# Optimization experiments

Hardware: AMD Instinct MI355X
Metric: run time of the kernel (lower is better)

The kernel has to match this reference:

```python
import jax, jax.numpy as jnp
import numpy as np

B, C, H, W = 8, 256, 128, 128
HEADS, WS = 8, 8
SHIFT = WS // 2  # type=='W' -> shift_size = window_size//2 in this repo
N = WS * WS


def _rel_pos_index(ws):
    coords = np.stack(np.meshgrid(np.arange(ws), np.arange(ws), indexing='ij')).reshape(2, -1)
    rel = (coords[:, :, None] - coords[:, None, :]).transpose(1, 2, 0)  # N,N,2
    rel[:, :, 0] += ws - 1
    rel[:, :, 1] += ws - 1
    rel[:, :, 0] *= 2 * ws - 1
    return rel.sum(-1)  # (N,N) ints in [0,(2ws-1)^2)


def _attn_mask(h, w, ws, shift):
    img = np.zeros((h, w), np.int32)
    cnt = 0
    for hs in (slice(0, -ws), slice(-ws, -shift), slice(-shift, None)):
        for wsl in (slice(0, -ws), slice(-ws, -shift), slice(-shift, None)):
            img[hs, wsl] = cnt
            cnt += 1
    m = img.reshape(h // ws, ws, w // ws, ws).transpose(0, 2, 1, 3).reshape(-1, ws * ws)
    diff = m[:, None, :] - m[:, :, None]
    return np.where(diff != 0, -100.0, 0.0).astype(np.float32)  # (nW,N,N)


def _ln(x, w, b, eps=1e-5):
    mu = jnp.mean(x, -1, keepdims=True)
    var = jnp.mean(jnp.square(x - mu), -1, keepdims=True)
    return (x - mu) * jax.lax.rsqrt(var + eps) * w + b


def setup_inputs() -> dict:
    key = jax.random.key(0)
    ks = jax.random.split(key, 10)
    s = 0.02
    return {
        'x': jax.random.normal(ks[0], (B, C, H, W), jnp.float32),
        'ln1_w': jnp.ones((C,), jnp.float32),
        'ln1_b': jnp.zeros((C,), jnp.float32),
        'qkv_w': jax.random.normal(ks[1], (3 * C, C), jnp.float32) * s,
        'qkv_b': jnp.zeros((3 * C,), jnp.float32),
        'rel_bias': jax.random.normal(ks[2], ((2 * WS - 1) ** 2, HEADS), jnp.float32) * s,
        'proj_w': jax.random.normal(ks[3], (C, C), jnp.float32) * s,
        'proj_b': jnp.zeros((C,), jnp.float32),
        'ln2_w': jnp.ones((C,), jnp.float32),
        'ln2_b': jnp.zeros((C,), jnp.float32),
        'fc1_w': jax.random.normal(ks[4], (4 * C, C), jnp.float32) * s,
        'fc1_b': jnp.zeros((4 * C,), jnp.float32),
        'fc2_w': jax.random.normal(ks[5], (C, 4 * C), jnp.float32) * s,
        'fc2_b': jnp.zeros((C,), jnp.float32),
    }


def reference(x, ln1_w, ln1_b, qkv_w, qkv_b, rel_bias, proj_w, proj_b,
              ln2_w, ln2_b, fc1_w, fc1_b, fc2_w, fc2_b):
    b, c, h, w = x.shape
    hd = c // HEADS
    scale = hd ** -0.5
    nW = (h // WS) * (w // WS)

    t = x.transpose(0, 2, 3, 1).reshape(b, h * w, c)  # b (hw) c
    shortcut = t
    t = _ln(t, ln1_w, ln1_b).reshape(b, h, w, c)
    t = jnp.roll(t, (-SHIFT, -SHIFT), axis=(1, 2))  # cyclic shift
    # window partition -> (b*nW, N, c)
    win = t.reshape(b, h // WS, WS, w // WS, WS, c).transpose(0, 1, 3, 2, 4, 5).reshape(b * nW, N, c)

    qkv = (win @ qkv_w.T + qkv_b).reshape(b * nW, N, 3, HEADS, hd).transpose(2, 0, 3, 1, 4)
    q, k, v = qkv[0], qkv[1], qkv[2]  # (b*nW, heads, N, hd)
    attn = jnp.einsum('bhnd,bhmd->bhnm', q * scale, k)
    rpi = jnp.asarray(_rel_pos_index(WS))
    bias = rel_bias[rpi.reshape(-1)].reshape(N, N, HEADS).transpose(2, 0, 1)  # (heads,N,N)
    attn = attn + bias[None]
    mask = jnp.asarray(_attn_mask(h, w, WS, SHIFT))  # (nW,N,N)
    attn = attn.reshape(b, nW, HEADS, N, N) + mask[None, :, None]
    attn = jax.nn.softmax(attn, axis=-1).reshape(b * nW, HEADS, N, N)
    out = jnp.einsum('bhnm,bhmd->bhnd', attn, v).transpose(0, 2, 1, 3).reshape(b * nW, N, c)
    out = out @ proj_w.T + proj_b
    # window reverse + reverse shift
    out = out.reshape(b, h // WS, w // WS, WS, WS, c).transpose(0, 1, 3, 2, 4, 5).reshape(b, h, w, c)
    out = jnp.roll(out, (SHIFT, SHIFT), axis=(1, 2)).reshape(b, h * w, c)

    t = shortcut + out
    h2 = _ln(t, ln2_w, ln2_b)
    h2 = jax.nn.gelu(h2 @ fc1_w.T + fc1_b)
    t = t + (h2 @ fc2_w.T + fc2_b)
    return t.reshape(b, h, w, c).transpose(0, 3, 1, 2)
```

## Files before the change

kernel.cpp:

```cpp
#include <hip/hip_runtime.h>
#include <cstdint>
#include <cstddef>

using f32x4 = __attribute__((ext_vector_type(4))) float;
using bf16x8 = __attribute__((ext_vector_type(8))) __bf16;
using u16x4 = __attribute__((ext_vector_type(4))) unsigned short;
using u16x8 = __attribute__((ext_vector_type(8))) unsigned short;

#define DEV __device__ __forceinline__

DEV unsigned short f2b(float f) {
  __bf16 h = (__bf16)f;
  return __builtin_bit_cast(unsigned short, h);
}
DEV float b2f(unsigned short u) {
  uint32_t w = ((uint32_t)u) << 16;
  return __builtin_bit_cast(float, w);
}

DEV void gload16(const unsigned short* g, unsigned short* l) {
  __builtin_amdgcn_global_load_lds(
      (const __attribute__((address_space(1))) void*)g,
      (__attribute__((address_space(3))) void*)l, 16, 0, 0);
}

DEV void waitv(int n) {
  switch (n) {
    case 0: asm volatile("s_waitcnt vmcnt(0)" ::: "memory"); break;
    case 2: asm volatile("s_waitcnt vmcnt(2)" ::: "memory"); break;
    case 8: asm volatile("s_waitcnt vmcnt(8)" ::: "memory"); break;
    default: asm volatile("s_waitcnt vmcnt(0)" ::: "memory"); break;
  }
}


__global__ void swin_cvt_all(const float* __restrict__ qkvw, const float* __restrict__ projw,
                             const float* __restrict__ fc1w, const float* __restrict__ fc2w,
                             unsigned short* __restrict__ wq, unsigned short* __restrict__ wp,
                             unsigned short* __restrict__ w1, unsigned short* __restrict__ w2,
                             const float* __restrict__ relb, float* __restrict__ bt) {
  int i = blockIdx.x * 256 + threadIdx.x;
  if (i < 196608) wq[i] = f2b(qkvw[i]);
  else if (i < 262144) wp[i - 196608] = f2b(projw[i - 196608]);
  else if (i < 524288) w1[i - 262144] = f2b(fc1w[i - 262144]);
  else if (i < 786432) w2[i - 524288] = f2b(fc2w[i - 524288]);
  else {
    int id = i - 786432;
    int m = id & 63, n = (id >> 6) & 63, head = (id >> 12) & 7, cls = id >> 15;
    bool eh = cls & 2, ew = cls & 1;
    int nh = n >> 3, nw = n & 7, mh = m >> 3, mw = m & 7;
    int rn = (eh ? ((nh >> 2) + 1) : 0) * 3 + (ew ? ((nw >> 2) + 1) : 0);
    int rm = (eh ? ((mh >> 2) + 1) : 0) * 3 + (ew ? ((mw >> 2) + 1) : 0);
    float v = relb[(size_t)((nh - mh + 7) * 15 + (nw - mw + 7)) * 8 + head];
    if (rn != rm) v -= 100.f;
    bt[id] = v;
  }
}

__global__ __launch_bounds__(256)
void swin_ln1win(const float* __restrict__ x,
                 const float* __restrict__ lw, const float* __restrict__ lb,
                 unsigned short* __restrict__ win, unsigned short* __restrict__ xb) {
  __shared__ float sh[512];
  __shared__ float mean_[128], rstd_[128];
  __shared__ unsigned short tile[128 * 260];
  int bh = blockIdx.x; int b = bh >> 7, h = bh & 127;
  int t = threadIdx.x;
  int w = t & 127, ch = t >> 7;
  const float* px = x + (((size_t)(b * 256 + ch * 128)) << 14) + (h << 7) + w;
  float s = 0.f, s2 = 0.f;
  for (int c = 0; c < 128; ++c) {
    float v = px[(size_t)c << 14];
    s += v; s2 += v * v;
    tile[w * 260 + ch * 128 + c] = f2b(v);
  }
  sh[t] = s; sh[256 + t] = s2;
  __syncthreads();
  if (ch == 0) {
    s += sh[t + 128]; s2 += sh[256 + t + 128];
    float mu = s * (1.f / 256.f);
    mean_[w] = mu;
    rstd_[w] = rsqrtf(s2 * (1.f / 256.f) - mu * mu + 1e-5f);
  }
  __syncthreads();
  int hp = (h + 124) & 127;
  int whh = hp >> 3, nh = hp & 7;
  int lg = t & 31, grp = t >> 5;
#pragma unroll
  for (int i = 0; i < 16; ++i) {
    int w2 = (i << 3) + grp;
    float mu = mean_[w2], rs = rstd_[w2];
    int wp_ = (w2 + 124) & 127;
    int wwc = wp_ >> 3, nw = wp_ & 7;
    size_t wt = (size_t)b * 256 + whh * 16 + wwc;
    int n = (nh << 3) + nw;
#pragma unroll
    for (int half = 0; half < 2; ++half) {
      int c = half * 128 + (lg << 2);
      u16x4 raw = *(const u16x4*)&tile[w2 * 260 + c];
      f32x4 lwv = *(const f32x4*)(lw + c);
      f32x4 lbv = *(const f32x4*)(lb + c);
      u16x4 o;
#pragma unroll
      for (int k = 0; k < 4; ++k)
        o[k] = f2b((b2f(raw[k]) - mu) * rs * lwv[k] + lbv[k]);
      *(u16x4*)&win[((wt << 6) + n) * 256 + c] = o;
      *(u16x4*)&xb[(((size_t)bh << 7) + w2) * 256 + c] = raw;
    }
  }
}

__global__ __launch_bounds__(512)
void swin_qkvattn(const unsigned short* __restrict__ win,
                  const unsigned short* __restrict__ wq,
                  const float* __restrict__ qkvb,
                  const float* __restrict__ btab,
                  unsigned short* __restrict__ attn_out) {
  __shared__ __align__(16) char L[133120];
  const int wt = blockIdx.x;
  const int t = threadIdx.x;
  const int lane = t & 63;
  const int head = t >> 6;
  const int cl = lane & 15, g = lane >> 4;

  {
    const unsigned short* src = win + (size_t)wt * 16384;
    int row = t >> 3;
    int sch = (t & 7) ^ (row & 7);
#pragma unroll
    for (int o = 0; o < 4; ++o)
      gload16(src + row * 256 + o * 64 + sch * 8,
              (unsigned short*)(L + o * 8192 + t * 16));
  }
  __syncthreads();

  f32x4 acc1[4][6] = {};
#pragma unroll
  for (int kt = 0; kt < 8; ++kt) {
    bf16x8 af[4], bf[6];
    const char* sub = L + (kt >> 1) * 8192;
    const int kc = (kt & 1) * 4 + g;
#pragma unroll
    for (int i = 0; i < 4; ++i) {
      int tok = i * 16 + cl;
      af[i] = *(const bf16x8*)(sub + tok * 128 + ((kc ^ (tok & 7)) * 16));
    }
#pragma unroll
    for (int j = 0; j < 6; ++j) {
      int col = (j >> 1) * 256 + head * 32 + (j & 1) * 16 + cl;
      bf[j] = *(const bf16x8*)(wq + (size_t)col * 256 + kt * 32 + g * 8);
    }
#pragma unroll
    for (int i = 0; i < 4; ++i)
#pragma unroll
      for (int j = 0; j < 6; ++j)
        acc1[i][j] = __builtin_amdgcn_mfma_f32_16x16x32_bf16(bf[j], af[i], acc1[i][j], 0, 0, 0);
  }

  char* hb = L + 32768 + head * 12544;
#pragma unroll
  for (int i = 0; i < 4; ++i) {
    int tok = i * 16 + cl;
#pragma unroll
    for (int j = 0; j < 6; ++j) {
      int p = j >> 1;
      int c32b = (j & 1) * 16 + (g << 2);
      f32x4 b4 = *(const f32x4*)(qkvb + p * 256 + head * 32 + c32b);
      if (p < 2) {
        u16x4 o;
#pragma unroll
        for (int r = 0; r < 4; ++r) {
          float v = acc1[i][j][r] + b4[r];
          if (p == 0) v *= 0.17677669529663687f;
          o[r] = f2b(v);
        }
        int chunk = ((j & 1) * 2 + (g >> 1)) ^ ((tok >> 1) & 3);
        *(u16x4*)(hb + p * 4096 + tok * 64 + chunk * 16 + (g & 1) * 8) = o;
      } else {
        unsigned short* vt = (unsigned short*)(hb + 8192);
#pragma unroll
        for (int r = 0; r < 4; ++r)
          vt[(c32b + r) * 68 + tok] = f2b(acc1[i][j][r] + b4[r]);
      }
    }
  }
  asm volatile("s_waitcnt lgkmcnt(0)" ::: "memory");
  __builtin_amdgcn_sched_barrier(0);

  bf16x8 qf[4], kf[4];
#pragma unroll
  for (int ni = 0; ni < 4; ++ni) {
    int tok = (ni << 4) + cl;
    int chunk = g ^ ((tok >> 1) & 3);
    qf[ni] = *(const bf16x8*)(hb + tok * 64 + chunk * 16);
    kf[ni] = *(const bf16x8*)(hb + 4096 + tok * 64 + chunk * 16);
  }
  f32x4 s[4][4] = {};
#pragma unroll
  for (int mi = 0; mi < 4; ++mi)
#pragma unroll
    for (int ni = 0; ni < 4; ++ni)
      s[mi][ni] = __builtin_amdgcn_mfma_f32_16x16x32_bf16(kf[mi], qf[ni], s[mi][ni], 0, 0, 0);

  int wi = wt & 255;
  int cls = (((wi >> 4) == 15) ? 2 : 0) + (((wi & 15) == 15) ? 1 : 0);
  const float* bt = btab + (((size_t)(cls << 3) + head) << 12);
#pragma unroll
  for (int ni = 0; ni < 4; ++ni) {
    int n = (ni << 4) + cl;
    float mx = -1e30f;
#pragma unroll
    for (int mi = 0; mi < 4; ++mi) {
      f32x4 bb = *(const f32x4*)&bt[n * 64 + (mi << 4) + (g << 2)];
#pragma unroll
      for (int r = 0; r < 4; ++r) {
        float v = s[mi][ni][r] + bb[r];
        s[mi][ni][r] = v;
        mx = fmaxf(mx, v);
      }
    }
    mx = fmaxf(mx, __shfl_xor(mx, 16));
    mx = fmaxf(mx, __shfl_xor(mx, 32));
    float sum = 0.f;
#pragma unroll
    for (int mi = 0; mi < 4; ++mi)
#pragma unroll
      for (int r = 0; r < 4; ++r) {
        float p = __expf(s[mi][ni][r] - mx);
        s[mi][ni][r] = p;
        sum += p;
      }
    sum += __shfl_xor(sum, 16);
    sum += __shfl_xor(sum, 32);
    float inv = __builtin_amdgcn_rcpf(sum);
#pragma unroll
    for (int mi = 0; mi < 4; ++mi) {
      u16x4 pk;
#pragma unroll
      for (int r = 0; r < 4; ++r) pk[r] = f2b(s[mi][ni][r] * inv);
      int chunk = (mi * 2 + (g >> 1)) ^ (n & 7);
      *(u16x4*)(hb + n * 128 + chunk * 16 + (g & 1) * 8) = pk;
    }
  }
  asm volatile("s_waitcnt lgkmcnt(0)" ::: "memory");
  __builtin_amdgcn_sched_barrier(0);

  union FragU { bf16x8 v; uint64_t q[2]; };
  f32x4 o[4][2] = {};
  const unsigned short* vt = (const unsigned short*)(hb + 8192);
#pragma unroll
  for (int mt = 0; mt < 2; ++mt) {
    FragU vf[2];
#pragma unroll
    for (int dt = 0; dt < 2; ++dt) {
      int d = (dt << 4) + cl;
      const unsigned short* p = vt + d * 68 + (mt << 5) + (g << 3);
      vf[dt].q[0] = *(const uint64_t*)p;
      vf[dt].q[1] = *(const uint64_t*)(p + 4);
    }
#pragma unroll
    for (int ni = 0; ni < 4; ++ni) {
      int n = (ni << 4) + cl;
      int chunk = (mt * 4 + g) ^ (n & 7);
      bf16x8 pa = *(const bf16x8*)(hb + n * 128 + chunk * 16);
#pragma unroll
      for (int dt = 0; dt < 2; ++dt)
        o[ni][dt] = __builtin_amdgcn_mfma_f32_16x16x32_bf16(pa, vf[dt].v, o[ni][dt], 0, 0, 0);
    }
  }

  int b = wt >> 8;
#pragma unroll
  for (int ni = 0; ni < 4; ++ni)
#pragma unroll
    for (int dt = 0; dt < 2; ++dt)
#pragma unroll
      for (int r = 0; r < 4; ++r) {
        int n = (ni << 4) + (g << 2) + r;
        int d = (dt << 4) + cl;
        int hs = ((wi >> 4) << 3) + (n >> 3), ws_ = ((wi & 15) << 3) + (n & 7);
        int hh = (hs + 4) & 127, ww = (ws_ + 4) & 127;
        size_t tok = ((size_t)b << 14) + (hh << 7) + ww;
        attn_out[tok * 256 + (head << 5) + d] = f2b(o[ni][dt][r]);
      }
}

__global__ __launch_bounds__(512, 2)
void swin_proj(const unsigned short* __restrict__ A,
               const unsigned short* __restrict__ Wt,
               const float* __restrict__ bias,
               unsigned short* __restrict__ T,
               const unsigned short* __restrict__ xb,
               const float* __restrict__ lw2, const float* __restrict__ lb2,
               unsigned short* __restrict__ tn) {
  constexpr int KT = 4;
  __shared__ __align__(16) unsigned short As[2][16384];
  __shared__ __align__(16) unsigned short Bs[2][16384];
  const int cpx = gridDim.x >> 3;
  const int bid = (blockIdx.x & 7) * cpx + (blockIdx.x >> 3);
  const int m0 = bid << 8;
  const int t = threadIdx.x;
  const int lane = t & 63;
  const int wave = t >> 6;
  const int wr = wave >> 2, wc = wave & 3;
  const int cl = lane & 15, g = lane >> 4;

  const int trow = t >> 3;
  const int ks = (t & 7) ^ (trow & 7);
  const unsigned short* agb = A  + (size_t)(m0 + trow) * 256 + ks * 8;
  const unsigned short* bgb = Wt + (size_t)trow * 256 + ks * 8;

  const int ra = wr * 128 + cl;
  const int rb = wc * 64 + cl;
  const int ka0 = (g ^ (cl & 7)) * 8;

  auto stage = [&](int buf, int kt) {
    const int ko = kt * 64;
#pragma unroll
    for (int l = 0; l < 4; ++l) {
      gload16(agb + (size_t)l * 64 * 256 + ko, &As[buf][l * 4096 + t * 8]);
      gload16(bgb + (size_t)l * 64 * 256 + ko, &Bs[buf][l * 4096 + t * 8]);
    }
  };

  f32x4 acc[8][4] = {};
  bf16x8 afA[8], bfA[4], afB[8], bfB[4];

  auto RD = [&](int buf, int kk, bf16x8* af, bf16x8* bfr) {
    const int ka = ka0 ^ (kk << 5);
#pragma unroll
    for (int i = 0; i < 8; ++i)
      af[i] = *(const bf16x8*)&As[buf][(ra + i * 16) * 64 + ka];
#pragma unroll
    for (int j = 0; j < 4; ++j)
      bfr[j] = *(const bf16x8*)&Bs[buf][(rb + j * 16) * 64 + ka];
  };
  auto MF = [&](bf16x8* af, bf16x8* bfr) {
    __builtin_amdgcn_s_setprio(1);
#pragma unroll
    for (int i = 0; i < 8; ++i)
#pragma unroll
      for (int j = 0; j < 4; ++j)
        acc[i][j] = __builtin_amdgcn_mfma_f32_16x16x32_bf16(bfr[j], af[i], acc[i][j], 0, 0, 0);
    __builtin_amdgcn_s_setprio(0);
  };

  stage(0, 0);
  stage(1, 1);
  waitv(8);
  __builtin_amdgcn_s_barrier();
  RD(0, 0, afA, bfA);
#pragma unroll
  for (int kt = 0; kt < KT; ++kt) {
    const int cur = kt & 1;
    RD(cur, 1, afB, bfB);
    MF(afA, bfA);
    asm volatile("s_waitcnt lgkmcnt(0)" ::: "memory");
    __builtin_amdgcn_sched_barrier(0);
    __builtin_amdgcn_s_barrier();
    if (kt + 2 < KT) stage(cur, kt + 2);
    if (kt + 1 < KT) waitv(8);
    else             waitv(0);
    __builtin_amdgcn_s_barrier();
    if (kt + 1 < KT) RD(cur ^ 1, 0, afA, bfA);
    MF(afB, bfB);
  }

  float s[8], s2v[8];
#pragma unroll
  for (int i = 0; i < 8; ++i) { s[i] = 0.f; s2v[i] = 0.f; }
#pragma unroll
  for (int i = 0; i < 8; ++i) {
    int row = m0 + wr * 128 + i * 16 + cl;
#pragma unroll
    for (int j = 0; j < 4; ++j) {
      int colb = wc * 64 + j * 16 + (g << 2);
      f32x4 b4 = *(const f32x4*)(bias + colb);
      u16x4 xv = *(const u16x4*)(xb + (size_t)row * 256 + colb);
#pragma unroll
      for (int r = 0; r < 4; ++r) {
        float v = acc[i][j][r] + b4[r] + b2f(xv[r]);
        acc[i][j][r] = v;
        s[i] += v; s2v[i] += v * v;
      }
    }
  }
#pragma unroll
  for (int i = 0; i < 8; ++i) {
    s[i]  += __shfl_xor(s[i], 16);  s[i]  += __shfl_xor(s[i], 32);
    s2v[i] += __shfl_xor(s2v[i], 16); s2v[i] += __shfl_xor(s2v[i], 32);
  }
  __syncthreads();
  float* lsum = (float*)&As[0][0];
  if (g == 0) {
#pragma unroll
    for (int i = 0; i < 8; ++i) {
      int rl = wr * 128 + i * 16 + cl;
      lsum[wc * 256 + rl] = s[i];
      lsum[1024 + wc * 256 + rl] = s2v[i];
    }
  }
  __syncthreads();
#pragma unroll
  for (int i = 0; i < 8; ++i) {
    int rl = wr * 128 + i * 16 + cl;
    float ts = lsum[rl] + lsum[256 + rl] + lsum[512 + rl] + lsum[768 + rl];
    float ts2 = lsum[1024 + rl] + lsum[1280 + rl] + lsum[1536 + rl] + lsum[1792 + rl];
    float mu = ts * (1.f / 256.f);
    float rstd = rsqrtf(ts2 * (1.f / 256.f) - mu * mu + 1e-5f);
    int row = m0 + rl;
#pragma unroll
    for (int j = 0; j < 4; ++j) {
      int colb = wc * 64 + j * 16 + (g << 2);
      f32x4 wv = *(const f32x4*)(lw2 + colb);
      f32x4 bv = *(const f32x4*)(lb2 + colb);
      u16x4 oT, on;
#pragma unroll
      for (int r = 0; r < 4; ++r) {
        float v = acc[i][j][r];
        oT[r] = f2b(v);
        on[r] = f2b((v - mu) * rstd * wv[r] + bv[r]);
      }
      *(u16x4*)(T + (size_t)row * 256 + colb) = oT;
      *(u16x4*)(tn + (size_t)row * 256 + colb) = on;
    }
  }
}

__global__ __launch_bounds__(512)
void swin_ffn(const unsigned short* __restrict__ tn,
              const unsigned short* __restrict__ w1,
              const unsigned short* __restrict__ w2,
              const float* __restrict__ b1,
              const float* __restrict__ b2,
              const unsigned short* __restrict__ T,
              float* __restrict__ out) {
  __shared__ __align__(16) unsigned short At[32768];
  __shared__ __align__(16) unsigned short Hs[32768];
  __shared__ __align__(16) unsigned short Bs[2][8192];
  const int cpx = gridDim.x >> 3;
  const int bid = (blockIdx.x & 7) * cpx + (blockIdx.x >> 3);
  const int m0 = bid << 7;
  const int t = threadIdx.x;
  const int lane = t & 63;
  const int wave = t >> 6;
  const int wr = wave >> 2, wc = wave & 3;
  const int cl = lane & 15, g = lane >> 4;

  const int arow = t >> 2;
  const int ks = (t & 3) ^ ((arow >> 1) & 3);
  const int ka = (g ^ ((cl >> 1) & 3)) * 8;
  const int ra = wr * 64 + cl;
  const int rb = wc * 64 + cl;

  auto stageB1 = [&](int buf, int q, int kt) {
    const unsigned short* wg = w1 + (size_t)(q * 256 + arow) * 256 + kt * 32 + ks * 8;
    gload16(wg, &Bs[buf][t * 8]);
    gload16(wg + 32768, &Bs[buf][4096 + t * 8]);
  };
  auto stageB2 = [&](int buf, int q, int kt) {
    const unsigned short* wg = w2 + (size_t)arow * 1024 + q * 256 + kt * 32 + ks * 8;
    gload16(wg, &Bs[buf][t * 8]);
    gload16(wg + 131072, &Bs[buf][4096 + t * 8]);
  };

  {
    int row0 = t >> 3;
    int ch = t & 7;
#pragma unroll
    for (int o = 0; o < 4; ++o)
#pragma unroll
      for (int p = 0; p < 2; ++p) {
        int row = p * 64 + row0;
        int sch = ch ^ (row & 7);
        gload16(tn + (size_t)(m0 + row) * 256 + o * 64 + sch * 8,
                &At[o * 8192 + (p * 512 + t) * 8]);
      }
  }

  f32x4 acc2[4][4] = {};

  for (int q = 0; q < 4; ++q) {
    f32x4 acc1[4][4] = {};
    stageB1(0, q, 0); stageB1(1, q, 1);
#pragma unroll
    for (int kt = 0; kt < 8; ++kt) {
      const int cur = kt & 1;
      waitv(kt < 7 ? 2 : 0);
      __builtin_amdgcn_s_barrier();
      bf16x8 af[4], bf[4];
#pragma unroll
      for (int i = 0; i < 4; ++i) {
        int row = ra + i * 16;
        int kc = ((kt & 1) * 4 + g) ^ (row & 7);
        af[i] = *(const bf16x8*)&At[(kt >> 1) * 8192 + row * 64 + kc * 8];
      }
#pragma unroll
      for (int j = 0; j < 4; ++j)
        bf[j] = *(const bf16x8*)&Bs[cur][(rb + j * 16) * 32 + ka];
      asm volatile("s_waitcnt lgkmcnt(0)" ::: "memory");
      __builtin_amdgcn_sched_barrier(0);
      __builtin_amdgcn_s_barrier();
      if (kt + 2 < 8) stageB1(cur, q, kt + 2);
      __builtin_amdgcn_s_setprio(1);
#pragma unroll
      for (int i = 0; i < 4; ++i)
#pragma unroll
        for (int j = 0; j < 4; ++j)
          acc1[i][j] = __builtin_amdgcn_mfma_f32_16x16x32_bf16(bf[j], af[i], acc1[i][j], 0, 0, 0);
      __builtin_amdgcn_s_setprio(0);
    }
    stageB2(0, q, 0); stageB2(1, q, 1);
#pragma unroll
    for (int i = 0; i < 4; ++i) {
      int row = wr * 64 + i * 16 + cl;
#pragma unroll
      for (int j = 0; j < 4; ++j) {
        f32x4 b4 = *(const f32x4*)(b1 + q * 256 + wc * 64 + j * 16 + (g << 2));
        u16x4 o;
#pragma unroll
        for (int r = 0; r < 4; ++r) {
          float v = acc1[i][j][r] + b4[r];
          float p = v * fmaf(v * v, -0.0713548256f, -1.5957691216f);
          float e = __expf(p);
          o[r] = f2b(v * __builtin_amdgcn_rcpf(1.f + e));
        }
        int chunk = (j * 2 + (g >> 1)) ^ (row & 7);
        *(u16x4*)((char*)Hs + wc * 16384 + row * 128 + chunk * 16 + (g & 1) * 8) = o;
      }
    }
    asm volatile("s_waitcnt lgkmcnt(0)" ::: "memory");
    __builtin_amdgcn_sched_barrier(0);
    __builtin_amdgcn_s_barrier();
#pragma unroll
    for (int kt = 0; kt < 8; ++kt) {
      const int cur = kt & 1;
      waitv(kt < 7 ? 2 : 0);
      __builtin_amdgcn_s_barrier();
      bf16x8 af2[4], bf2[4];
#pragma unroll
      for (int i = 0; i < 4; ++i) {
        int row = ra + i * 16;
        int kc = ((kt & 1) * 4 + g) ^ (row & 7);
        af2[i] = *(const bf16x8*)&Hs[(kt >> 1) * 8192 + row * 64 + kc * 8];
      }
#pragma unroll
      for (int j = 0; j < 4; ++j)
        bf2[j] = *(const bf16x8*)&Bs[cur][(rb + j * 16) * 32 + ka];
      asm volatile("s_waitcnt lgkmcnt(0)" ::: "memory");
      __builtin_amdgcn_sched_barrier(0);
      __builtin_amdgcn_s_barrier();
      if (kt + 2 < 8) stageB2(cur, q, kt + 2);
      __builtin_amdgcn_s_setprio(1);
#pragma unroll
      for (int i = 0; i < 4; ++i)
#pragma unroll
        for (int j = 0; j < 4; ++j)
          acc2[i][j] = __builtin_amdgcn_mfma_f32_16x16x32_bf16(bf2[j], af2[i], acc2[i][j], 0, 0, 0);
      __builtin_amdgcn_s_setprio(0);
    }
  }

#pragma unroll
  for (int i = 0; i < 4; ++i) {
    int row = m0 + wr * 64 + i * 16 + cl;
    int b = row >> 14, hw = row & 16383;
#pragma unroll
    for (int j = 0; j < 4; ++j) {
      int colb = wc * 64 + j * 16 + (g << 2);
      f32x4 b4 = *(const f32x4*)(b2 + colb);
      u16x4 tv = *(const u16x4*)(T + (size_t)row * 256 + colb);
#pragma unroll
      for (int r = 0; r < 4; ++r)
        out[((size_t)(b * 256 + colb + r) << 14) + hw] = acc2[i][j][r] + b4[r] + b2f(tv[r]);
    }
  }
}

extern "C" void kernel_launch(void* const* d_in, const int* in_sizes, int n_in,
                              void* d_out, int out_size, void* d_ws, size_t ws_size,
                              hipStream_t stream) {
  const float* x    = (const float*)d_in[0];
  const float* ln1w = (const float*)d_in[1];
  const float* ln1b = (const float*)d_in[2];
  const float* qkvw = (const float*)d_in[3];
  const float* qkvb = (const float*)d_in[4];
  const float* relb = (const float*)d_in[5];
  const float* projw = (const float*)d_in[6];
  const float* projb = (const float*)d_in[7];
  const float* ln2w = (const float*)d_in[8];
  const float* ln2b = (const float*)d_in[9];
  const float* fc1w = (const float*)d_in[10];
  const float* fc1b = (const float*)d_in[11];
  const float* fc2w = (const float*)d_in[12];
  const float* fc2b = (const float*)d_in[13];

  char* ws = (char*)d_ws;
  unsigned short* win      = (unsigned short*)(ws);
  unsigned short* attn_out = (unsigned short*)(ws + 67108864);
  unsigned short* tn       = (unsigned short*)(ws + 134217728);
  unsigned short* T        = (unsigned short*)(ws + 268435456);
  unsigned short* xb       = (unsigned short*)(ws + 335544320);
  unsigned short* wq  = (unsigned short*)(ws + 402653184);
  unsigned short* wp  = (unsigned short*)(ws + 403046400);
  unsigned short* w1  = (unsigned short*)(ws + 403177472);
  unsigned short* w2  = (unsigned short*)(ws + 403701760);
  float* btab         = (float*)(ws + 404226048);

  if (ws_size < 404750336ull) return;

  swin_cvt_all<<<3584, 256, 0, stream>>>(qkvw, projw, fc1w, fc2w, wq, wp, w1, w2, relb, btab);
  swin_ln1win<<<1024, 256, 0, stream>>>(x, ln1w, ln1b, win, xb);
  swin_qkvattn<<<2048, 512, 0, stream>>>(win, wq, qkvb, btab, attn_out);
  swin_proj<<<512, 512, 0, stream>>>(attn_out, wp, projb, T, xb, ln2w, ln2b, tn);
  swin_ffn<<<1024, 512, 0, stream>>>(tn, w1, w2, fc1b, fc2b, T, (float*)d_out);
}
```

Baseline: 514.6 us.

## Read FFN weight fragments directly from global memory instead of staging in LDS

The FFN kernel no longer stages weight tiles through a double-buffered LDS buffer. Each wave now loads its B fragments straight from global memory (served by L2), which removes the per-k-step barriers and frees 32KB of LDS. Launch bounds now request two blocks per CU, so the freed LDS and the register cap can raise occupancy. The cost is that every wave issues uncoalesced, latency-exposed global loads with no prefetch, and the register cap may cause spills.

```diff
diff --git a/kernel.cpp b/kernel.cpp
--- a/kernel.cpp
+++ b/kernel.cpp
@@ -427,7 +427,7 @@
   }
 }
 
-__global__ __launch_bounds__(512)
+__global__ __launch_bounds__(512, 2)
 void swin_ffn(const unsigned short* __restrict__ tn,
               const unsigned short* __restrict__ w1,
               const unsigned short* __restrict__ w2,
@@ -437,7 +437,6 @@
               float* __restrict__ out) {
   __shared__ __align__(16) unsigned short At[32768];
   __shared__ __align__(16) unsigned short Hs[32768];
-  __shared__ __align__(16) unsigned short Bs[2][8192];
   const int cpx = gridDim.x >> 3;
   const int bid = (blockIdx.x & 7) * cpx + (blockIdx.x >> 3);
   const int m0 = bid << 7;
@@ -446,23 +445,8 @@
   const int wave = t >> 6;
   const int wr = wave >> 2, wc = wave & 3;
   const int cl = lane & 15, g = lane >> 4;
-
-  const int arow = t >> 2;
-  const int ks = (t & 3) ^ ((arow >> 1) & 3);
-  const int ka = (g ^ ((cl >> 1) & 3)) * 8;
   const int ra = wr * 64 + cl;
   const int rb = wc * 64 + cl;
-
-  auto stageB1 = [&](int buf, int q, int kt) {
-    const unsigned short* wg = w1 + (size_t)(q * 256 + arow) * 256 + kt * 32 + ks * 8;
-    gload16(wg, &Bs[buf][t * 8]);
-    gload16(wg + 32768, &Bs[buf][4096 + t * 8]);
-  };
-  auto stageB2 = [&](int buf, int q, int kt) {
-    const unsigned short* wg = w2 + (size_t)arow * 1024 + q * 256 + kt * 32 + ks * 8;
-    gload16(wg, &Bs[buf][t * 8]);
-    gload16(wg + 131072, &Bs[buf][4096 + t * 8]);
-  };
 
   {
     int row0 = t >> 3;
@@ -477,17 +461,17 @@
                 &At[o * 8192 + (p * 512 + t) * 8]);
       }
   }
+  waitv(0);
+  __builtin_amdgcn_s_barrier();
 
   f32x4 acc2[4][4] = {};
+  const unsigned short* w1b = w1 + (size_t)rb * 256;
+  const unsigned short* w2b = w2 + (size_t)rb * 1024;
 
   for (int q = 0; q < 4; ++q) {
     f32x4 acc1[4][4] = {};
-    stageB1(0, q, 0); stageB1(1, q, 1);
 #pragma unroll
     for (int kt = 0; kt < 8; ++kt) {
-      const int cur = kt & 1;
-      waitv(kt < 7 ? 2 : 0);
-      __builtin_amdgcn_s_barrier();
       bf16x8 af[4], bf[4];
 #pragma unroll
       for (int i = 0; i < 4; ++i) {
@@ -497,20 +481,14 @@
       }
 #pragma unroll
       for (int j = 0; j < 4; ++j)
-        bf[j] = *(const bf16x8*)&Bs[cur][(rb + j * 16) * 32 + ka];
-      asm volatile("s_waitcnt lgkmcnt(0)" ::: "memory");
-      __builtin_amdgcn_sched_barrier(0);
-      __builtin_amdgcn_s_barrier();
-      if (kt + 2 < 8) stageB1(cur, q, kt + 2);
-      __builtin_amdgcn_s_setprio(1);
+        bf[j] = *(const bf16x8*)(w1b + (size_t)(q * 256 + j * 16) * 256 + kt * 32 + g * 8);
 #pragma unroll
       for (int i = 0; i < 4; ++i)
 #pragma unroll
         for (int j = 0; j < 4; ++j)
           acc1[i][j] = __builtin_amdgcn_mfma_f32_16x16x32_bf16(bf[j], af[i], acc1[i][j], 0, 0, 0);
-      __builtin_amdgcn_s_setprio(0);
-    }
-    stageB2(0, q, 0); stageB2(1, q, 1);
+    }
+    __builtin_amdgcn_s_barrier();
 #pragma unroll
     for (int i = 0; i < 4; ++i) {
       int row = wr * 64 + i * 16 + cl;
@@ -534,9 +512,6 @@
     __builtin_amdgcn_s_barrier();
 #pragma unroll
     for (int kt = 0; kt < 8; ++kt) {
-      const int cur = kt & 1;
-      waitv(kt < 7 ? 2 : 0);
-      __builtin_amdgcn_s_barrier();
       bf16x8 af2[4], bf2[4];
 #pragma unroll
       for (int i = 0; i < 4; ++i) {
@@ -546,18 +521,12 @@
       }
 #pragma unroll
       for (int j = 0; j < 4; ++j)
-        bf2[j] = *(const bf16x8*)&Bs[cur][(rb + j * 16) * 32 + ka];
-      asm volatile("s_waitcnt lgkmcnt(0)" ::: "memory");
-      __builtin_amdgcn_sched_barrier(0);
-      __builtin_amdgcn_s_barrier();
-      if (kt + 2 < 8) stageB2(cur, q, kt + 2);
-      __builtin_amdgcn_s_setprio(1);
+        bf2[j] = *(const bf16x8*)(w2b + (size_t)(j * 16) * 1024 + q * 256 + kt * 32 + g * 8);
 #pragma unroll
       for (int i = 0; i < 4; ++i)
 #pragma unroll
         for (int j = 0; j < 4; ++j)
           acc2[i][j] = __builtin_amdgcn_mfma_f32_16x16x32_bf16(bf2[j], af2[i], acc2[i][j], 0, 0, 0);
-      __builtin_amdgcn_s_setprio(0);
     }
   }
 
```

Result: slower. 633.0 us (+23.0%).

## Use per-wave private weight staging in FFN to drop block barriers

Applied to the files above, without the earlier changes.

Each wave now stages its own slice of the fc1/fc2 weight tiles into a private LDS region and waits only on its own loads. This removes the two block-wide barriers per k-step. The GELU hidden buffer is halved and filled in two phases, with barriers only at the midpoint, so that LDS use stays within limits. In exchange, each weight tile is fetched redundantly by the two wave rows, and more GELU values are held in registers.

```diff
diff --git a/kernel.cpp b/kernel.cpp
--- a/kernel.cpp
+++ b/kernel.cpp
@@ -28,6 +28,7 @@
   switch (n) {
     case 0: asm volatile("s_waitcnt vmcnt(0)" ::: "memory"); break;
     case 2: asm volatile("s_waitcnt vmcnt(2)" ::: "memory"); break;
+    case 4: asm volatile("s_waitcnt vmcnt(4)" ::: "memory"); break;
     case 8: asm volatile("s_waitcnt vmcnt(8)" ::: "memory"); break;
     default: asm volatile("s_waitcnt vmcnt(0)" ::: "memory"); break;
   }
@@ -436,8 +437,8 @@
               const unsigned short* __restrict__ T,
               float* __restrict__ out) {
   __shared__ __align__(16) unsigned short At[32768];
-  __shared__ __align__(16) unsigned short Hs[32768];
-  __shared__ __align__(16) unsigned short Bs[2][8192];
+  __shared__ __align__(16) unsigned short Hs[16384];
+  __shared__ __align__(16) unsigned short Bw[32768];
   const int cpx = gridDim.x >> 3;
   const int bid = (blockIdx.x & 7) * cpx + (blockIdx.x >> 3);
   const int m0 = bid << 7;
@@ -446,22 +447,27 @@
   const int wave = t >> 6;
   const int wr = wave >> 2, wc = wave & 3;
   const int cl = lane & 15, g = lane >> 4;
-
-  const int arow = t >> 2;
-  const int ks = (t & 3) ^ ((arow >> 1) & 3);
+  const int ra = wr * 64 + cl;
   const int ka = (g ^ ((cl >> 1) & 3)) * 8;
-  const int ra = wr * 64 + cl;
-  const int rb = wc * 64 + cl;
+  unsigned short* bwb = Bw + wave * 4096;
+  const int srow = lane >> 2;
+  const int skc = (lane & 3) ^ ((lane >> 3) & 3);
 
   auto stageB1 = [&](int buf, int q, int kt) {
-    const unsigned short* wg = w1 + (size_t)(q * 256 + arow) * 256 + kt * 32 + ks * 8;
-    gload16(wg, &Bs[buf][t * 8]);
-    gload16(wg + 32768, &Bs[buf][4096 + t * 8]);
+    unsigned short* dst = bwb + buf * 2048;
+#pragma unroll
+    for (int p = 0; p < 4; ++p) {
+      int row = q * 256 + wc * 64 + p * 16 + srow;
+      gload16(w1 + (size_t)row * 256 + kt * 32 + skc * 8, dst + p * 512 + lane * 8);
+    }
   };
   auto stageB2 = [&](int buf, int q, int kt) {
-    const unsigned short* wg = w2 + (size_t)arow * 1024 + q * 256 + kt * 32 + ks * 8;
-    gload16(wg, &Bs[buf][t * 8]);
-    gload16(wg + 131072, &Bs[buf][4096 + t * 8]);
+    unsigned short* dst = bwb + buf * 2048;
+#pragma unroll
+    for (int p = 0; p < 4; ++p) {
+      int row = wc * 64 + p * 16 + srow;
+      gload16(w2 + (size_t)row * 1024 + q * 256 + kt * 32 + skc * 8, dst + p * 512 + lane * 8);
+    }
   };
 
   {
@@ -481,13 +487,16 @@
   f32x4 acc2[4][4] = {};
 
   for (int q = 0; q < 4; ++q) {
+    stageB1(0, q, 0); stageB1(1, q, 1);
+    if (q == 0) {
+      waitv(8);
+      __builtin_amdgcn_s_barrier();
+    }
     f32x4 acc1[4][4] = {};
-    stageB1(0, q, 0); stageB1(1, q, 1);
 #pragma unroll
     for (int kt = 0; kt < 8; ++kt) {
       const int cur = kt & 1;
-      waitv(kt < 7 ? 2 : 0);
-      __builtin_amdgcn_s_barrier();
+      waitv(kt < 7 ? 4 : 0);
       bf16x8 af[4], bf[4];
 #pragma unroll
       for (int i = 0; i < 4; ++i) {
@@ -497,10 +506,9 @@
       }
 #pragma unroll
       for (int j = 0; j < 4; ++j)
-        bf[j] = *(const bf16x8*)&Bs[cur][(rb + j * 16) * 32 + ka];
+        bf[j] = *(const bf16x8*)&bwb[cur * 2048 + (j * 16 + cl) * 32 + ka];
       asm volatile("s_waitcnt lgkmcnt(0)" ::: "memory");
       __builtin_amdgcn_sched_barrier(0);
-      __builtin_amdgcn_s_barrier();
       if (kt + 2 < 8) stageB1(cur, q, kt + 2);
       __builtin_amdgcn_s_setprio(1);
 #pragma unroll
@@ -510,47 +518,62 @@
           acc1[i][j] = __builtin_amdgcn_mfma_f32_16x16x32_bf16(bf[j], af[i], acc1[i][j], 0, 0, 0);
       __builtin_amdgcn_s_setprio(0);
     }
-    stageB2(0, q, 0); stageB2(1, q, 1);
-#pragma unroll
-    for (int i = 0; i < 4; ++i) {
-      int row = wr * 64 + i * 16 + cl;
+    u16x4 gv[4][4];
+#pragma unroll
+    for (int i = 0; i < 4; ++i)
 #pragma unroll
       for (int j = 0; j < 4; ++j) {
         f32x4 b4 = *(const f32x4*)(b1 + q * 256 + wc * 64 + j * 16 + (g << 2));
-        u16x4 o;
 #pragma unroll
         for (int r = 0; r < 4; ++r) {
           float v = acc1[i][j][r] + b4[r];
           float p = v * fmaf(v * v, -0.0713548256f, -1.5957691216f);
           float e = __expf(p);
-          o[r] = f2b(v * __builtin_amdgcn_rcpf(1.f + e));
+          gv[i][j][r] = f2b(v * __builtin_amdgcn_rcpf(1.f + e));
         }
-        int chunk = (j * 2 + (g >> 1)) ^ (row & 7);
-        *(u16x4*)((char*)Hs + wc * 16384 + row * 128 + chunk * 16 + (g & 1) * 8) = o;
-      }
-    }
+      }
+    stageB2(0, q, 0); stageB2(1, q, 1);
+    auto writeGelu = [&]() {
+#pragma unroll
+      for (int i = 0; i < 4; ++i) {
+        int row = wr * 64 + i * 16 + cl;
+#pragma unroll
+        for (int j = 0; j < 4; ++j) {
+          int chunk = (j * 2 + (g >> 1)) ^ (row & 7);
+          *(u16x4*)((char*)Hs + (wc & 1) * 16384 + row * 128 + chunk * 16 + (g & 1) * 8) = gv[i][j];
+        }
+      }
+    };
+    __builtin_amdgcn_s_barrier();
+    if ((wc >> 1) == 0) writeGelu();
     asm volatile("s_waitcnt lgkmcnt(0)" ::: "memory");
     __builtin_amdgcn_sched_barrier(0);
     __builtin_amdgcn_s_barrier();
 #pragma unroll
-    for (int kt = 0; kt < 8; ++kt) {
-      const int cur = kt & 1;
-      waitv(kt < 7 ? 2 : 0);
-      __builtin_amdgcn_s_barrier();
+    for (int kt2 = 0; kt2 < 8; ++kt2) {
+      if (kt2 == 4) {
+        __builtin_amdgcn_s_barrier();
+        if ((wc >> 1) == 1) writeGelu();
+        asm volatile("s_waitcnt lgkmcnt(0)" ::: "memory");
+        __builtin_amdgcn_sched_barrier(0);
+        __builtin_amdgcn_s_barrier();
+      }
+      const int cur = kt2 & 1;
+      const int ktl = kt2 & 3;
+      waitv(kt2 < 7 ? 4 : 0);
       bf16x8 af2[4], bf2[4];
 #pragma unroll
       for (int i = 0; i < 4; ++i) {
         int row = ra + i * 16;
-        int kc = ((kt & 1) * 4 + g) ^ (row & 7);
-        af2[i] = *(const bf16x8*)&Hs[(kt >> 1) * 8192 + row * 64 + kc * 8];
+        int kc = ((ktl & 1) * 4 + g) ^ (row & 7);
+        af2[i] = *(const bf16x8*)&Hs[(ktl >> 1) * 8192 + row * 64 + kc * 8];
       }
 #pragma unroll
       for (int j = 0; j < 4; ++j)
-        bf2[j] = *(const bf16x8*)&Bs[cur][(rb + j * 16) * 32 + ka];
+        bf2[j] = *(const bf16x8*)&bwb[cur * 2048 + (j * 16 + cl) * 32 + ka];
       asm volatile("s_waitcnt lgkmcnt(0)" ::: "memory");
       __builtin_amdgcn_sched_barrier(0);
-      __builtin_amdgcn_s_barrier();
-      if (kt + 2 < 8) stageB2(cur, q, kt + 2);
+      if (kt2 + 2 < 8) stageB2(cur, q, kt2 + 2);
       __builtin_amdgcn_s_setprio(1);
 #pragma unroll
       for (int i = 0; i < 4; ++i)
```

Result: no change. 515.9 us (+0.2%).
